# Performance work log

Hardware: AMD Instinct MI355X
Metric: run time of the kernel (lower is better)

The kernel has to match this reference:

```python
import jax, jax.numpy as jnp
import numpy as np

N = 200_000   # nodes per component
E = 400_000   # directed edges per component
F_IN = 32     # raw node features
H = 96        # hidden_dim / GatedGraphConv out_channels
L = 6         # num_layers inside GatedGraphConv
B = 4096      # number of molecules (graphs) in batch
FC = 4 * H    # 384


def _gru_cell(m, h, w_ih, w_hh, b_ih, b_hh):
    # torch.nn.GRUCell math; w_* are [3H, H], b_* are [3H]
    gi = m @ w_ih.T + b_ih
    gh = h @ w_hh.T + b_hh
    i_r, i_z, i_n = jnp.split(gi, 3, axis=1)
    h_r, h_z, h_n = jnp.split(gh, 3, axis=1)
    r = jax.nn.sigmoid(i_r + h_r)
    z = jax.nn.sigmoid(i_z + h_z)
    n = jnp.tanh(i_n + r * h_n)
    return (1.0 - z) * n + z * h


def _gated_graph_conv(x, edge_index, W, w_ih, w_hh, b_ih, b_hh):
    n_nodes = x.shape[0]
    h = jnp.pad(x, ((0, 0), (0, H - x.shape[1])))  # pad features to H
    src, dst = edge_index[0], edge_index[1]        # message flows src -> dst
    for i in range(L):
        m = h @ W[i]                                # [N, H]
        agg = jax.ops.segment_sum(m[src], dst, num_segments=n_nodes)
        h = _gru_cell(agg, h, w_ih, w_hh, b_ih, b_hh)
    return h


def _pool_component(x, edge_index, batch, W, w_ih, w_hh, b_ih, b_hh):
    h = jax.nn.relu(_gated_graph_conv(x, edge_index, W, w_ih, w_hh, b_ih, b_hh))
    sums = jax.ops.segment_sum(h, batch, num_segments=B)
    cnt = jax.ops.segment_sum(jnp.ones((h.shape[0], 1), h.dtype), batch, num_segments=B)
    return sums / jnp.maximum(cnt, 1.0)            # global_mean_pool -> [B, H]


def setup_inputs() -> dict:
    key = jax.random.key(0)
    ks = jax.random.split(key, 16)
    d = {}
    for i in range(3):
        c = str(i + 1)
        kx, ke, kb = jax.random.split(ks[i], 3)
        d['x' + c] = jax.random.normal(kx, (N, F_IN), jnp.float32)
        d['edge_index' + c] = jax.random.randint(ke, (2, E), 0, N)
        d['batch' + c] = jnp.sort(jax.random.randint(kb, (N,), 0, B))
        kw = jax.random.split(ks[3 + i], 5)
        d['W' + c] = jax.random.normal(kw[0], (L, H, H), jnp.float32) * 0.05
        d['wih' + c] = jax.random.normal(kw[1], (3 * H, H), jnp.float32) * 0.05
        d['whh' + c] = jax.random.normal(kw[2], (3 * H, H), jnp.float32) * 0.05
        d['bih' + c] = jax.random.normal(kw[3], (3 * H,), jnp.float32) * 0.05
        d['bhh' + c] = jax.random.normal(kw[4], (3 * H,), jnp.float32) * 0.05
    kf = jax.random.split(ks[7], 6)
    d['fc1_w'] = jax.random.normal(kf[0], (FC, FC * 4), jnp.float32) * 0.05
    d['fc1_b'] = jnp.zeros((FC * 4,), jnp.float32)
    d['fc2_w'] = jax.random.normal(kf[1], (FC * 4, FC), jnp.float32) * 0.05
    d['fc2_b'] = jnp.zeros((FC,), jnp.float32)
    d['fc3_w'] = jax.random.normal(kf[2], (FC, 3), jnp.float32) * 0.05
    d['fc3_b'] = jnp.zeros((3,), jnp.float32)
    return d


def reference(x1, edge_index1, batch1, x2, edge_index2, batch2, x3, edge_index3, batch3,
              W1, wih1, whh1, bih1, bhh1,
              W2, wih2, whh2, bih2, bhh2,
              W3, wih3, whh3, bih3, bhh3,
              fc1_w, fc1_b, fc2_w, fc2_b, fc3_w, fc3_b):
    g1 = _pool_component(x1, edge_index1, batch1, W1, wih1, whh1, bih1, bhh1)
    g2 = _pool_component(x2, edge_index2, batch2, W2, wih2, whh2, bih2, bhh2)
    g3 = _pool_component(x3, edge_index3, batch3, W3, wih3, whh3, bih3, bhh3)
    xx = g1 * g2 * g3
    x = jnp.concatenate((g1, g2, g3, xx), axis=1)   # [B, 4H]
    x = jax.nn.relu(x @ fc1_w + fc1_b)              # dropout is identity (eval)
    x = jax.nn.relu(x @ fc2_w + fc2_b)
    return x @ fc3_w + fc3_b                        # [B, 3]
```

## Files before the change

kernel.cpp:

```cpp
#include <hip/hip_runtime.h>
#include <math.h>

#define NN_ 200000
#define EE_ 400000
#define HH  96
#define LL  6
#define BB  4096
#define NT_ 12500
#define SCAN_B 1024
#define NB_SCAN 196

typedef short s8v __attribute__((ext_vector_type(8)));
typedef float f4v __attribute__((ext_vector_type(4)));
typedef float f2v __attribute__((ext_vector_type(2)));

static inline int cdiv(int a, int b) { return (a + b - 1) / b; }

__device__ __forceinline__ float sigmoidf_(float x) { return 1.0f / (1.0f + __expf(-x)); }
__device__ __forceinline__ float tanhf_(float x) { return 1.0f - 2.0f / (__expf(2.0f * x) + 1.0f); }
__device__ __forceinline__ unsigned short f2bf(float x) {
    unsigned u = __float_as_uint(x);
    unsigned r = u + 0x7FFF + ((u >> 16) & 1);
    return (unsigned short)(r >> 16);
}
__device__ __forceinline__ float bf2f(unsigned short u) {
    return __uint_as_float(((unsigned)u) << 16);
}
__device__ __forceinline__ s8v load_bf8(const float* __restrict__ p) {
    float4 v0 = *(const float4*)p;
    float4 v1 = *(const float4*)(p + 4);
    s8v r;
    r[0] = (short)f2bf(v0.x); r[1] = (short)f2bf(v0.y);
    r[2] = (short)f2bf(v0.z); r[3] = (short)f2bf(v0.w);
    r[4] = (short)f2bf(v1.x); r[5] = (short)f2bf(v1.y);
    r[6] = (short)f2bf(v1.z); r[7] = (short)f2bf(v1.w);
    return r;
}

__device__ __forceinline__ void accu_(f2v& a, unsigned u) {
    a[0] += __uint_as_float(u << 16);
    a[1] += __uint_as_float(u & 0xFFFF0000u);
}
__device__ __forceinline__ void acc_row_(f2v* ag2, const uint4& u, int ks) {
    accu_(ag2[ks * 4 + 0], u.x); accu_(ag2[ks * 4 + 1], u.y);
    accu_(ag2[ks * 4 + 2], u.z); accu_(ag2[ks * 4 + 3], u.w);
}

__global__ void packB_k(const float* __restrict__ B, unsigned short* __restrict__ Bp,
                        int K, int N)
{
    int idx = blockIdx.x * 256 + threadIdx.x;
    if (idx >= K * N) return;
    int k = idx / N, n = idx % N;
    Bp[(((size_t)(k >> 5) * N + n) * 4 + ((k >> 3) & 3)) * 8 + (k & 7)] = f2bf(B[idx]);
}

__global__ void wfuse_k(const float* __restrict__ W, const float* __restrict__ wih,
                        float* __restrict__ wf)
{
    int idx = blockIdx.x * 256 + threadIdx.x;
    if (idx >= LL * 96 * 288) return;
    int l = idx / (96 * 288);
    int r = idx - l * 96 * 288;
    int k = r / 288;
    int g = r - k * 288;
    const float* wr = W + (size_t)l * 9216 + (size_t)k * 96;
    const float* vr = wih + (size_t)g * 96;
    float s = 0.f;
    #pragma unroll 8
    for (int j = 0; j < 96; j++) s += wr[j] * vr[j];
    wf[idx] = s;
}

__global__ void packWgf_k(const float* __restrict__ wf, const float* __restrict__ whh,
                          unsigned short* __restrict__ Wgf)
{
    int idx = blockIdx.x * 256 + threadIdx.x;
    if (idx >= LL * 6 * 18 * 64 * 8) return;
    int l = idx / 55296;
    int r = idx - l * 55296;
    int j    = r & 7;
    int lane = (r >> 3) & 63;
    int rest = r >> 9;
    int ksb = rest % 18;
    int jb  = rest / 18;
    int quad = lane >> 4, lc = lane & 15;
    int g, ks;
    if (ksb < 6)       { g = 0; ks = ksb; }
    else if (ksb < 12) { g = 1; ks = ksb - 6; }
    else if (ksb < 15) { g = 2; ks = ksb - 12; }
    else               { g = 3; ks = ksb - 12; }
    int k = ks * 32 + quad * 8 + j;
    int n = g * 96 + jb * 16 + lc;
    float v;
    if (n < 288) {
        v = (k < 96) ? wf[(size_t)l * 27648 + (size_t)k * 288 + n]
                     : whh[(size_t)n * 96 + (k - 96)];
    } else {
        v = whh[(size_t)(192 + (n - 288)) * 96 + (k - 96)];
    }
    Wgf[idx] = f2bf(v);
}

__global__ void bpack_k(const float* __restrict__ bih, const float* __restrict__ bhh,
                        float* __restrict__ bs)
{
    int j = threadIdx.x;
    if (j >= 96) return;
    bs[j]        = bih[j] + bhh[j];
    bs[96 + j]   = bih[96 + j] + bhh[96 + j];
    bs[192 + j]  = bih[192 + j];
    bs[288 + j]  = bhh[192 + j];
}

__global__ void pad_k(const float* __restrict__ x, unsigned short* __restrict__ hbf)
{
    int idx = blockIdx.x * 256 + threadIdx.x;
    if (idx >= NN_ * HH) return;
    int n = idx / HH, j = idx % HH;
    float v = (j < 32) ? x[n * 32 + j] : 0.f;
    hbf[idx] = f2bf(v);
}

__global__ void deg_k(const int* __restrict__ ei, int* __restrict__ deg)
{
    int e = blockIdx.x * 256 + threadIdx.x;
    if (e >= EE_) return;
    atomicAdd(&deg[ei[EE_ + e]], 1);
}

__global__ __launch_bounds__(SCAN_B) void scan1_k(
    const int* __restrict__ deg, int* __restrict__ rp, int* __restrict__ bsum)
{
    __shared__ int sh[SCAN_B];
    int i = blockIdx.x * SCAN_B + threadIdx.x;
    int v = (i < NN_) ? deg[i] : 0;
    sh[threadIdx.x] = v;
    __syncthreads();
    for (int off = 1; off < SCAN_B; off <<= 1) {
        int t = (threadIdx.x >= off) ? sh[threadIdx.x - off] : 0;
        __syncthreads();
        sh[threadIdx.x] += t;
        __syncthreads();
    }
    if (i < NN_) rp[i] = sh[threadIdx.x] - v;
    if (threadIdx.x == SCAN_B - 1) bsum[blockIdx.x] = sh[threadIdx.x];
}

__global__ __launch_bounds__(256) void scan2_k(int* __restrict__ bsum)
{
    __shared__ int sh[256];
    int v = (threadIdx.x < NB_SCAN) ? bsum[threadIdx.x] : 0;
    sh[threadIdx.x] = v;
    __syncthreads();
    for (int off = 1; off < 256; off <<= 1) {
        int t = (threadIdx.x >= off) ? sh[threadIdx.x - off] : 0;
        __syncthreads();
        sh[threadIdx.x] += t;
        __syncthreads();
    }
    if (threadIdx.x < NB_SCAN) bsum[threadIdx.x] = sh[threadIdx.x] - v;
}

__global__ void scan3_k(int* __restrict__ rp, const int* __restrict__ bsum,
                        int* __restrict__ cur)
{
    int i = blockIdx.x * 256 + threadIdx.x;
    if (i < NN_) {
        int r = rp[i] + bsum[i / SCAN_B];
        rp[i] = r;
        cur[i] = r;
    }
    if (i == 0) rp[NN_] = EE_;
}

__global__ void fill_k(const int* __restrict__ ei, int* __restrict__ cur,
                       int* __restrict__ srcs)
{
    int e = blockIdx.x * 256 + threadIdx.x;
    if (e >= EE_) return;
    int s = ei[e];
    int d = ei[EE_ + e];
    int pos = atomicAdd(&cur[d], 1);
    srcs[pos] = s * 192;
}

__global__ void brp_k(const int* __restrict__ bat, int* __restrict__ rpb)
{
    int i = blockIdx.x * 256 + threadIdx.x;
    if (i >= NN_) return;
    int b = bat[i];
    if (i == 0) {
        for (int q = 0; q <= b; q++) rpb[q] = 0;
    } else {
        int p = bat[i - 1];
        for (int q = p + 1; q <= b; q++) rpb[q] = i;
    }
    if (i == NN_ - 1) {
        for (int q = b + 1; q <= BB; q++) rpb[q] = NN_;
    }
}

__global__ __launch_bounds__(128) void agg_k(
    const int* __restrict__ rp, const int* __restrict__ srcs,
    const unsigned short* __restrict__ hbf,
    unsigned short* __restrict__ aggbf)
{
    int tid  = threadIdx.x;
    int wave = tid >> 6;
    int lane = tid & 63;
    int quad = lane >> 4;
    int lc   = lane & 15;
    int nT0  = blockIdx.x * 4 + wave * 2;

    const char* gbase = (const char*)hbf + quad * 16;

    #pragma unroll
    for (int t = 0; t < 2; t++) {
        int node = (nT0 + t) * 16 + lc;
        f2v ag2[12];
        #pragma unroll
        for (int i = 0; i < 12; i++) ag2[i] = (f2v){0.f, 0.f};
        int e = rp[node], e1 = rp[node + 1];
        for (; e < e1; e++) {
            const char* r = gbase + srcs[e];
            uint4 u0 = *(const uint4*)r;
            uint4 u1 = *(const uint4*)(r + 64);
            uint4 u2 = *(const uint4*)(r + 128);
            acc_row_(ag2, u0, 0); acc_row_(ag2, u1, 1); acc_row_(ag2, u2, 2);
        }
        #pragma unroll
        for (int ks = 0; ks < 3; ks++) {
            unsigned q0 = (unsigned)f2bf(ag2[ks * 4 + 0][0]) | ((unsigned)f2bf(ag2[ks * 4 + 0][1]) << 16);
            unsigned q1 = (unsigned)f2bf(ag2[ks * 4 + 1][0]) | ((unsigned)f2bf(ag2[ks * 4 + 1][1]) << 16);
            unsigned q2 = (unsigned)f2bf(ag2[ks * 4 + 2][0]) | ((unsigned)f2bf(ag2[ks * 4 + 2][1]) << 16);
            unsigned q3 = (unsigned)f2bf(ag2[ks * 4 + 3][0]) | ((unsigned)f2bf(ag2[ks * 4 + 3][1]) << 16);
            *(uint4*)(aggbf + (size_t)node * 96 + ks * 32 + quad * 8) =
                make_uint4(q0, q1, q2, q3);
        }
    }
}

__global__ __launch_bounds__(512) void gru_k(
    const unsigned short* __restrict__ aggbf,
    const unsigned short* __restrict__ Wgf,
    const float* __restrict__ bs,
    const unsigned short* __restrict__ hbf_prev,
    unsigned short* __restrict__ hbf_next,
    float* __restrict__ h,
    int writeH)
{
    __shared__ unsigned short lw[27648];
    int tid  = threadIdx.x;
    int part = blockIdx.y;

    {
        const uint4* src = (const uint4*)Wgf + (size_t)part * 3456;
        uint4* dst = (uint4*)lw;
        #pragma unroll
        for (int it = 0; it < 7; it++) {
            int i = it * 512 + tid;
            if (i < 3456) dst[i] = src[i];
        }
    }
    __syncthreads();

    int wave = tid >> 6;
    int lane = tid & 63;
    int quad = lane >> 4;
    int lc   = lane & 15;
    int nT0  = blockIdx.x * 16 + wave * 2;

    bool val[2];
    val[0] = (nT0 + 0) < NT_;
    val[1] = (nT0 + 1) < NT_;

    s8v z8;
    #pragma unroll
    for (int q = 0; q < 8; q++) z8[q] = 0;

    s8v d[2][6];
    #pragma unroll
    for (int t = 0; t < 2; t++) {
        int node = (nT0 + t) * 16 + lc;
        #pragma unroll
        for (int ks = 0; ks < 3; ks++) {
            if (val[t]) {
                d[t][ks]     = *(const s8v*)(aggbf    + (size_t)node * 96 + ks * 32 + quad * 8);
                d[t][3 + ks] = *(const s8v*)(hbf_prev + (size_t)node * 96 + ks * 32 + quad * 8);
            } else {
                d[t][ks]     = z8;
                d[t][3 + ks] = z8;
            }
        }
    }

    for (int jbl = 0; jbl < 3; jbl++) {
        int jb = part * 3 + jbl;
        uint2 hu[2];
        #pragma unroll
        for (int t = 0; t < 2; t++) {
            if (val[t])
                hu[t] = *(const uint2*)(hbf_prev + (size_t)((nT0 + t) * 16 + lc) * 96 + jb * 16 + quad * 4);
            else
                hu[t] = make_uint2(0u, 0u);
        }
        f4v acc[2][4] = {};
        const unsigned short* wj = lw + (size_t)jbl * 18 * 512 + (size_t)lane * 8;
        #pragma unroll
        for (int ks = 0; ks < 6; ks++) {
            s8v w = *(const s8v*)(wj + ks * 512);
            acc[0][0] = __builtin_amdgcn_mfma_f32_16x16x32_bf16(w, d[0][ks], acc[0][0], 0, 0, 0);
            acc[1][0] = __builtin_amdgcn_mfma_f32_16x16x32_bf16(w, d[1][ks], acc[1][0], 0, 0, 0);
        }
        #pragma unroll
        for (int ks = 0; ks < 6; ks++) {
            s8v w = *(const s8v*)(wj + (6 + ks) * 512);
            acc[0][1] = __builtin_amdgcn_mfma_f32_16x16x32_bf16(w, d[0][ks], acc[0][1], 0, 0, 0);
            acc[1][1] = __builtin_amdgcn_mfma_f32_16x16x32_bf16(w, d[1][ks], acc[1][1], 0, 0, 0);
        }
        #pragma unroll
        for (int ks = 0; ks < 6; ks++) {
            s8v w = *(const s8v*)(wj + (12 + ks) * 512);
            int g = (ks < 3) ? 2 : 3;
            acc[0][g] = __builtin_amdgcn_mfma_f32_16x16x32_bf16(w, d[0][ks], acc[0][g], 0, 0, 0);
            acc[1][g] = __builtin_amdgcn_mfma_f32_16x16x32_bf16(w, d[1][ks], acc[1][g], 0, 0, 0);
        }
        const float* bp = bs + jb * 16 + quad * 4;
        float4 br  = *(const float4*)(bp);
        float4 bz  = *(const float4*)(bp + 96);
        float4 bin = *(const float4*)(bp + 192);
        float4 bhn = *(const float4*)(bp + 288);
        float brv[4]  = {br.x, br.y, br.z, br.w};
        float bzv[4]  = {bz.x, bz.y, bz.z, bz.w};
        float binv[4] = {bin.x, bin.y, bin.z, bin.w};
        float bhnv[4] = {bhn.x, bhn.y, bhn.z, bhn.w};
        #pragma unroll
        for (int t = 0; t < 2; t++) {
            if (!val[t]) continue;
            int node = (nT0 + t) * 16 + lc;
            float hv[4];
            hv[0] = bf2f((unsigned short)(hu[t].x & 0xFFFF));
            hv[1] = bf2f((unsigned short)(hu[t].x >> 16));
            hv[2] = bf2f((unsigned short)(hu[t].y & 0xFFFF));
            hv[3] = bf2f((unsigned short)(hu[t].y >> 16));
            float out[4];
            #pragma unroll
            for (int i = 0; i < 4; i++) {
                float rg = sigmoidf_(acc[t][0][i] + brv[i]);
                float zg = sigmoidf_(acc[t][1][i] + bzv[i]);
                float nn = tanhf_(acc[t][2][i] + binv[i] + rg * (acc[t][3][i] + bhnv[i]));
                out[i] = (1.f - zg) * nn + zg * hv[i];
            }
            unsigned short q0 = f2bf(out[0]), q1 = f2bf(out[1]);
            unsigned short q2 = f2bf(out[2]), q3 = f2bf(out[3]);
            *(uint2*)(hbf_next + (size_t)node * 96 + jb * 16 + quad * 4) =
                make_uint2((unsigned)q0 | ((unsigned)q1 << 16),
                           (unsigned)q2 | ((unsigned)q3 << 16));
            if (writeH) {
                float* hp = h + (size_t)node * 96 + jb * 16 + quad * 4;
                *(float4*)hp = make_float4(out[0], out[1], out[2], out[3]);
            }
        }
    }
}

__global__ __launch_bounds__(128) void pool_csr_k(
    const float* __restrict__ h, const int* __restrict__ rpb, float* __restrict__ g)
{
    int b = blockIdx.x;
    int j = threadIdx.x;
    if (j >= 96) return;
    int n0 = rpb[b], n1 = rpb[b + 1];
    float s = 0.f;
    for (int n = n0; n < n1; n++) s += fmaxf(h[(size_t)n * 96 + j], 0.f);
    float c = (float)(n1 - n0);
    g[(size_t)b * 96 + j] = s / fmaxf(c, 1.f);
}

__global__ void feat_k(const float* __restrict__ g1, const float* __restrict__ g2,
                       const float* __restrict__ g3, float* __restrict__ feat)
{
    int idx = blockIdx.x * 256 + threadIdx.x;
    if (idx >= BB * HH) return;
    int b = idx / HH, j = idx % HH;
    float a = g1[idx], bb = g2[idx], c = g3[idx];
    float* f = feat + (size_t)b * 384;
    f[j]       = a;
    f[96 + j]  = bb;
    f[192 + j] = c;
    f[288 + j] = a * bb * c;
}

__global__ __launch_bounds__(256) void gemm_mlp_mfma(
    const float* __restrict__ A, const unsigned short* __restrict__ Bp,
    const float* __restrict__ bias, float* __restrict__ C,
    int K, int N, int doRelu)
{
    int wave = threadIdx.x >> 6;
    int lane = threadIdx.x & 63;
    int quad = lane >> 4;
    int lc   = lane & 15;
    int rowA = blockIdx.y * 16 + lc;
    int colb = blockIdx.x * 128 + wave * 32;

    f4v acc[2] = {};
    for (int ks = 0; ks < K / 32; ks++) {
        s8v a = load_bf8(A + (size_t)rowA * K + ks * 32 + quad * 8);
        #pragma unroll
        for (int t = 0; t < 2; t++) {
            int n = colb + t * 16 + lc;
            s8v b = *(const s8v*)(Bp + ((size_t)(ks * N + n) * 4 + quad) * 8);
            acc[t] = __builtin_amdgcn_mfma_f32_16x16x32_bf16(a, b, acc[t], 0, 0, 0);
        }
    }
    int rowD = blockIdx.y * 16 + quad * 4;
    #pragma unroll
    for (int t = 0; t < 2; t++) {
        int n = colb + t * 16 + lc;
        float bv = bias[n];
        #pragma unroll
        for (int r = 0; r < 4; r++) {
            float v = acc[t][r] + bv;
            if (doRelu) v = fmaxf(v, 0.f);
            C[(size_t)(rowD + r) * N + n] = v;
        }
    }
}

__global__ __launch_bounds__(256) void fc3_k(const float* __restrict__ t2,
                                             const float* __restrict__ w,
                                             const float* __restrict__ bias,
                                             float* __restrict__ out)
{
    int wave = threadIdx.x >> 6;
    int lane = threadIdx.x & 63;
    int b = blockIdx.x * 4 + wave;
    const float* row = t2 + (size_t)b * 384;
    float a0 = 0.f, a1 = 0.f, a2 = 0.f;
    #pragma unroll
    for (int kk = 0; kk < 6; kk++) {
        int k = kk * 64 + lane;
        float x = row[k];
        a0 += x * w[k * 3 + 0];
        a1 += x * w[k * 3 + 1];
        a2 += x * w[k * 3 + 2];
    }
    #pragma unroll
    for (int off = 32; off > 0; off >>= 1) {
        a0 += __shfl_down(a0, off);
        a1 += __shfl_down(a1, off);
        a2 += __shfl_down(a2, off);
    }
    if (lane == 0) {
        out[b * 3 + 0] = a0 + bias[0];
        out[b * 3 + 1] = a1 + bias[1];
        out[b * 3 + 2] = a2 + bias[2];
    }
}

extern "C" void kernel_launch(void* const* d_in, const int* in_sizes, int n_in,
                              void* d_out, int out_size, void* d_ws, size_t ws_size,
                              hipStream_t stream)
{
    float* ws    = (float*)d_ws;
    float* h     = ws;
    float* hbfAF = h + (size_t)NN_ * HH;
    float* hbfBF = hbfAF + (size_t)NN_ * HH / 2;
    float* aggF  = hbfBF + (size_t)NN_ * HH / 2;
    float* wfF   = aggF + (size_t)NN_ * HH / 2;
    float* wgfF  = wfF + 165888;
    float* fc1pF = wgfF + 165888;
    float* fc2pF = fc1pF + 294912;
    float* g3    = fc2pF + 294912;
    int*   rp    = (int*)(g3 + 3 * (size_t)BB * HH);
    int*   srcs  = rp + 200064;
    int*   deg   = srcs + 400000;
    int*   cur   = deg + 200000;
    int*   bsum  = cur + 200000;
    int*   rpb   = bsum + 256;
    float* bs    = (float*)(rpb + 4097) + 1;

    unsigned short* hbfA = (unsigned short*)hbfAF;
    unsigned short* hbfB = (unsigned short*)hbfBF;
    unsigned short* agg  = (unsigned short*)aggF;
    unsigned short* Wgf  = (unsigned short*)wgfF;
    unsigned short* fc1p = (unsigned short*)fc1pF;
    unsigned short* fc2p = (unsigned short*)fc2pF;

    float* feat = h;
    float* t1   = h + 2 * 1024 * 1024;
    float* t2   = h + 9 * 1024 * 1024;

    for (int c = 0; c < 3; c++) {
        const float* x   = (const float*)d_in[c * 8 + 0];
        const int*   ei  = (const int*)  d_in[c * 8 + 1];
        const int*   bat = (const int*)  d_in[c * 8 + 2];
        const float* W   = (const float*)d_in[c * 8 + 3];
        const float* wih = (const float*)d_in[c * 8 + 4];
        const float* whh = (const float*)d_in[c * 8 + 5];
        const float* bih = (const float*)d_in[c * 8 + 6];
        const float* bhh = (const float*)d_in[c * 8 + 7];

        hipMemsetAsync(deg, 0, NN_ * sizeof(int), stream);
        deg_k<<<cdiv(EE_, 256), 256, 0, stream>>>(ei, deg);
        scan1_k<<<NB_SCAN, SCAN_B, 0, stream>>>(deg, rp, bsum);
        scan2_k<<<1, 256, 0, stream>>>(bsum);
        scan3_k<<<cdiv(NN_, 256), 256, 0, stream>>>(rp, bsum, cur);
        fill_k<<<cdiv(EE_, 256), 256, 0, stream>>>(ei, cur, srcs);
        brp_k<<<cdiv(NN_, 256), 256, 0, stream>>>(bat, rpb);

        wfuse_k<<<cdiv(LL * 96 * 288, 256), 256, 0, stream>>>(W, wih, wfF);
        packWgf_k<<<cdiv(LL * 6 * 18 * 64 * 8, 256), 256, 0, stream>>>(wfF, whh, Wgf);
        bpack_k<<<1, 128, 0, stream>>>(bih, bhh, bs);
        pad_k<<<cdiv(NN_ * HH, 256), 256, 0, stream>>>(x, hbfA);

        unsigned short* pb[2] = {hbfA, hbfB};
        for (int l = 0; l < LL; l++) {
            agg_k<<<NN_ / 64, 128, 0, stream>>>(rp, srcs, pb[l & 1], agg);
            gru_k<<<dim3(cdiv(NT_, 16), 2), 512, 0, stream>>>(
                agg, Wgf + (size_t)l * 55296, bs, pb[l & 1], pb[(l + 1) & 1],
                h, (l == LL - 1) ? 1 : 0);
        }

        pool_csr_k<<<BB, 128, 0, stream>>>(h, rpb, g3 + (size_t)c * BB * HH);
    }

    const float* fc1_w = (const float*)d_in[24];
    const float* fc1_b = (const float*)d_in[25];
    const float* fc2_w = (const float*)d_in[26];
    const float* fc2_b = (const float*)d_in[27];
    const float* fc3_w = (const float*)d_in[28];
    const float* fc3_b = (const float*)d_in[29];

    packB_k<<<cdiv(384 * 1536, 256), 256, 0, stream>>>(fc1_w, fc1p, 384, 1536);
    packB_k<<<cdiv(1536 * 384, 256), 256, 0, stream>>>(fc2_w, fc2p, 1536, 384);

    feat_k<<<cdiv(BB * HH, 256), 256, 0, stream>>>(
        g3, g3 + (size_t)BB * HH, g3 + 2 * (size_t)BB * HH, feat);
    gemm_mlp_mfma<<<dim3(1536 / 128, BB / 16), 256, 0, stream>>>(
        feat, fc1p, fc1_b, t1, 384, 1536, 1);
    gemm_mlp_mfma<<<dim3(384 / 128, BB / 16), 256, 0, stream>>>(
        t1, fc2p, fc2_b, t2, 1536, 384, 1);
    fc3_k<<<BB / 4, 256, 0, stream>>>(t2, fc3_w, fc3_b, (float*)d_out);
}
```

Measured before the change: 2.288 ms.

## Fuse edge aggregation into GRU kernel, removing the agg buffer round-trip

Merges the CSR gather-sum kernel into the GRU/MFMA kernel, so each wave aggregates its own nodes' neighbor rows in registers and feeds them straight to the MFMAs. This removes the bf16 agg buffer write and re-read and one kernel launch per layer. The weight-to-LDS copy is now overlapped with the gather by moving the barrier after aggregation. The trade-off is that the gather is done twice, once per blockIdx.y part (grid y=2), doubling random neighbor reads, and gather latency now sits inside a large-LDS, 512-thread block.

```diff
diff --git a/kernel.cpp b/kernel.cpp
--- a/kernel.cpp
+++ b/kernel.cpp
@@ -201,48 +201,8 @@
     }
 }
 
-__global__ __launch_bounds__(128) void agg_k(
+__global__ __launch_bounds__(512) void layer_k(
     const int* __restrict__ rp, const int* __restrict__ srcs,
-    const unsigned short* __restrict__ hbf,
-    unsigned short* __restrict__ aggbf)
-{
-    int tid  = threadIdx.x;
-    int wave = tid >> 6;
-    int lane = tid & 63;
-    int quad = lane >> 4;
-    int lc   = lane & 15;
-    int nT0  = blockIdx.x * 4 + wave * 2;
-
-    const char* gbase = (const char*)hbf + quad * 16;
-
-    #pragma unroll
-    for (int t = 0; t < 2; t++) {
-        int node = (nT0 + t) * 16 + lc;
-        f2v ag2[12];
-        #pragma unroll
-        for (int i = 0; i < 12; i++) ag2[i] = (f2v){0.f, 0.f};
-        int e = rp[node], e1 = rp[node + 1];
-        for (; e < e1; e++) {
-            const char* r = gbase + srcs[e];
-            uint4 u0 = *(const uint4*)r;
-            uint4 u1 = *(const uint4*)(r + 64);
-            uint4 u2 = *(const uint4*)(r + 128);
-            acc_row_(ag2, u0, 0); acc_row_(ag2, u1, 1); acc_row_(ag2, u2, 2);
-        }
-        #pragma unroll
-        for (int ks = 0; ks < 3; ks++) {
-            unsigned q0 = (unsigned)f2bf(ag2[ks * 4 + 0][0]) | ((unsigned)f2bf(ag2[ks * 4 + 0][1]) << 16);
-            unsigned q1 = (unsigned)f2bf(ag2[ks * 4 + 1][0]) | ((unsigned)f2bf(ag2[ks * 4 + 1][1]) << 16);
-            unsigned q2 = (unsigned)f2bf(ag2[ks * 4 + 2][0]) | ((unsigned)f2bf(ag2[ks * 4 + 2][1]) << 16);
-            unsigned q3 = (unsigned)f2bf(ag2[ks * 4 + 3][0]) | ((unsigned)f2bf(ag2[ks * 4 + 3][1]) << 16);
-            *(uint4*)(aggbf + (size_t)node * 96 + ks * 32 + quad * 8) =
-                make_uint4(q0, q1, q2, q3);
-        }
-    }
-}
-
-__global__ __launch_bounds__(512) void gru_k(
-    const unsigned short* __restrict__ aggbf,
     const unsigned short* __restrict__ Wgf,
     const float* __restrict__ bs,
     const unsigned short* __restrict__ hbf_prev,
@@ -263,7 +223,6 @@
             if (i < 3456) dst[i] = src[i];
         }
     }
-    __syncthreads();
 
     int wave = tid >> 6;
     int lane = tid & 63;
@@ -279,21 +238,46 @@
     #pragma unroll
     for (int q = 0; q < 8; q++) z8[q] = 0;
 
+    int n0 = nT0 * 16 + lc;
+    int e0t[2] = {0, 0}, e1t[2] = {0, 0};
+    if (val[0]) { e0t[0] = rp[n0];      e1t[0] = rp[n0 + 1]; }
+    if (val[1]) { e0t[1] = rp[n0 + 16]; e1t[1] = rp[n0 + 17]; }
+
+    const char* gbase = (const char*)hbf_prev + quad * 16;
+
     s8v d[2][6];
     #pragma unroll
     for (int t = 0; t < 2; t++) {
+        f2v ag2[12];
+        #pragma unroll
+        for (int i = 0; i < 12; i++) ag2[i] = (f2v){0.f, 0.f};
+        for (int e = e0t[t]; e < e1t[t]; e++) {
+            const char* r = gbase + srcs[e];
+            uint4 u0 = *(const uint4*)r;
+            uint4 u1 = *(const uint4*)(r + 64);
+            uint4 u2 = *(const uint4*)(r + 128);
+            acc_row_(ag2, u0, 0); acc_row_(ag2, u1, 1); acc_row_(ag2, u2, 2);
+        }
+        #pragma unroll
+        for (int ks = 0; ks < 3; ks++) {
+            s8v v;
+            #pragma unroll
+            for (int w = 0; w < 4; w++) {
+                v[2 * w]     = (short)f2bf(ag2[ks * 4 + w][0]);
+                v[2 * w + 1] = (short)f2bf(ag2[ks * 4 + w][1]);
+            }
+            d[t][ks] = v;
+        }
         int node = (nT0 + t) * 16 + lc;
         #pragma unroll
         for (int ks = 0; ks < 3; ks++) {
-            if (val[t]) {
-                d[t][ks]     = *(const s8v*)(aggbf    + (size_t)node * 96 + ks * 32 + quad * 8);
-                d[t][3 + ks] = *(const s8v*)(hbf_prev + (size_t)node * 96 + ks * 32 + quad * 8);
-            } else {
-                d[t][ks]     = z8;
-                d[t][3 + ks] = z8;
-            }
-        }
-    }
+            d[t][3 + ks] = val[t]
+                ? *(const s8v*)(hbf_prev + (size_t)node * 96 + ks * 32 + quad * 8)
+                : z8;
+        }
+    }
+
+    __syncthreads();
 
     for (int jbl = 0; jbl < 3; jbl++) {
         int jb = part * 3 + jbl;
@@ -467,8 +451,7 @@
     float* h     = ws;
     float* hbfAF = h + (size_t)NN_ * HH;
     float* hbfBF = hbfAF + (size_t)NN_ * HH / 2;
-    float* aggF  = hbfBF + (size_t)NN_ * HH / 2;
-    float* wfF   = aggF + (size_t)NN_ * HH / 2;
+    float* wfF   = hbfBF + (size_t)NN_ * HH / 2;
     float* wgfF  = wfF + 165888;
     float* fc1pF = wgfF + 165888;
     float* fc2pF = fc1pF + 294912;
@@ -483,7 +466,6 @@
 
     unsigned short* hbfA = (unsigned short*)hbfAF;
     unsigned short* hbfB = (unsigned short*)hbfBF;
-    unsigned short* agg  = (unsigned short*)aggF;
     unsigned short* Wgf  = (unsigned short*)wgfF;
     unsigned short* fc1p = (unsigned short*)fc1pF;
     unsigned short* fc2p = (unsigned short*)fc2pF;
@@ -517,9 +499,8 @@
 
         unsigned short* pb[2] = {hbfA, hbfB};
         for (int l = 0; l < LL; l++) {
-            agg_k<<<NN_ / 64, 128, 0, stream>>>(rp, srcs, pb[l & 1], agg);
-            gru_k<<<dim3(cdiv(NT_, 16), 2), 512, 0, stream>>>(
-                agg, Wgf + (size_t)l * 55296, bs, pb[l & 1], pb[(l + 1) & 1],
+            layer_k<<<dim3(cdiv(NT_, 16), 2), 512, 0, stream>>>(
+                rp, srcs, Wgf + (size_t)l * 55296, bs, pb[l & 1], pb[(l + 1) & 1],
                 h, (l == LL - 1) ? 1 : 0);
         }
 
```

Result: no change. 2.282 ms (-0.3%).
